# Performance work log

Measured on AMD Instinct MI355X. Metric: run time of the kernel, lower is better.

Reference implementation:

```python
import jax, jax.numpy as jnp
import numpy as np

B, D, H, W = 32, 256, 32, 32
K = 1024

def setup_inputs() -> dict:
    key = jax.random.key(0)
    k1, k2 = jax.random.split(key)
    x = jax.random.normal(k1, (B, D, H, W), dtype=jnp.float32)
    codebook = jax.random.normal(k2, (K, D), dtype=jnp.float32)
    return {"x": x, "codebook": codebook}

def reference(x, codebook):
    b, lat, h, w = x.shape
    # (B, D, H, W) -> (B*H*W, D) tokens
    xt = jnp.transpose(x, (0, 2, 3, 1)).reshape(-1, lat)  # [N, D]
    # Squared euclidean distances via expansion (argmin-equivalent to cdist)
    x_sq = jnp.sum(xt * xt, axis=-1, keepdims=True)           # [N, 1]
    c_sq = jnp.sum(codebook * codebook, axis=-1)[None, :]     # [1, K]
    dist2 = x_sq - 2.0 * (xt @ codebook.T) + c_sq             # [N, K]
    idx = jnp.argmin(dist2, axis=-1)                          # [N]
    quant = codebook[idx]                                     # [N, D]
    codebook_loss = jnp.mean((jax.lax.stop_gradient(xt) - quant) ** 2)
    commitment_loss = jnp.mean((xt - jax.lax.stop_gradient(quant)) ** 2)
    # Straight-through estimator
    out = xt + jax.lax.stop_gradient(quant - xt)              # [N, D]
    out = out.reshape(b, h, w, lat).transpose(0, 3, 1, 2)     # [B, D, H, W]
    min_enc_idx = idx.reshape(b, h, w)                        # [B, H, W]
    return out, min_enc_idx, codebook_loss, commitment_loss
```

## Files before the change

kernel.cpp:

```cpp
#include <hip/hip_runtime.h>

#define B_   32
#define D_   256
#define HW_  1024
#define N_   32768
#define K_   1024
#define DHW  (D_ * HW_)
#define MARGIN 0.3f

typedef __attribute__((ext_vector_type(8)))  short bf16x8;
typedef __attribute__((ext_vector_type(16))) float f32x16;

union FragU { uint4 q; bf16x8 v; };

__device__ inline uint bf16rne(float x) {
    uint ub = __float_as_uint(x);
    return (ub + 0x7fffu + ((ub >> 16) & 1u)) >> 16;
}

__global__ __launch_bounds__(256)
void prep_cb(const float* __restrict__ cb, uint4* __restrict__ cbt2,
             float* __restrict__ csq, float* __restrict__ cbT,
             int* __restrict__ rcount, float* __restrict__ oloss) {
    __shared__ uint sh[256], sl[256];
    __shared__ float rr[4];
    const int k = blockIdx.x, d = threadIdx.x;
    float v = cb[(size_t)k * D_ + d];
    uint hb = bf16rne(v);
    float hf = __uint_as_float(hb << 16);
    uint lb = bf16rne(v - hf);
    sh[d] = hb; sl[d] = lb;
    cbT[(size_t)d * K_ + k] = v;
    float s = v * v;
    #pragma unroll
    for (int off = 32; off >= 1; off >>= 1) s += __shfl_xor(s, off, 64);
    if ((d & 63) == 0) rr[d >> 6] = s;
    __syncthreads();
    if (d == 0) csq[k] = (rr[0] + rr[1]) + (rr[2] + rr[3]);
    if (k == 0 && d == 0) { *rcount = 0; oloss[0] = 0.f; oloss[1] = 0.f; }
    if (d < 64) {
        const int ch = d >> 2, it = d & 3;
        const int p = it >> 1, h = it & 1;
        const int d0 = ch * 16 + h * 8;
        const uint* src = p ? sl : sh;
        uint w[4];
        #pragma unroll
        for (int jj = 0; jj < 4; ++jj)
            w[jj] = src[d0 + 2 * jj] | (src[d0 + 2 * jj + 1] << 16);
        cbt2[((ch * 4 + it) << 10) + k] = make_uint4(w[0], w[1], w[2], w[3]);
    }
}

#define DO_STEP(SA, SB, SC, SD, S) do {                                          \
    const int cc_ = cq * 4 + (S);                                                \
    const int ch_ = cc_ & 15;                                                    \
    FragU tf[4];                                                                 \
    _Pragma("unroll")                                                            \
    for (int j = 0; j < 4; ++j) tf[j].q = TkS[ch_ * 2 + sub][j * 32 + l31];      \
    __builtin_amdgcn_s_setprio(1);                                               \
    _Pragma("unroll")                                                            \
    for (int j = 0; j < 4; ++j)                                                  \
        acc[0][j] = __builtin_amdgcn_mfma_f32_32x32x16_bf16(SA.v, tf[j].v, acc[0][j], 0, 0, 0); \
    _Pragma("unroll")                                                            \
    for (int j = 0; j < 4; ++j)                                                  \
        acc[1][j] = __builtin_amdgcn_mfma_f32_32x32x16_bf16(SB.v, tf[j].v, acc[1][j], 0, 0, 0); \
    _Pragma("unroll")                                                            \
    for (int j = 0; j < 4; ++j)                                                  \
        acc[0][j] = __builtin_amdgcn_mfma_f32_32x32x16_bf16(SC.v, tf[j].v, acc[0][j], 0, 0, 0); \
    _Pragma("unroll")                                                            \
    for (int j = 0; j < 4; ++j)                                                  \
        acc[1][j] = __builtin_amdgcn_mfma_f32_32x32x16_bf16(SD.v, tf[j].v, acc[1][j], 0, 0, 0); \
    __builtin_amdgcn_s_setprio(0);                                               \
    if (cq < 7) {                                                                \
        const int nc_ = cc_ + 4;                                                 \
        const int noff_ = (((nc_ & 15) * 4) << 10) + ((nc_ >> 4) * 64);          \
        SA.q = cb_hi[noff_];      SB.q = cb_hi[noff_ + 32];                      \
        SC.q = cb_lo[noff_];      SD.q = cb_lo[noff_ + 32];                      \
    }                                                                            \
} while (0)

__global__ __launch_bounds__(512, 1)
void vq_main(const float* __restrict__ x, const uint4* __restrict__ cbt2,
             const float* __restrict__ csqg, const float* __restrict__ cb,
             int* __restrict__ rcount, int* __restrict__ rlist,
             float* __restrict__ bdist, float* __restrict__ out,
             float* __restrict__ oidx, float* __restrict__ oloss) {
    __shared__ __align__(16) uint SMEM[17408];
    uint4 (*TkS)[128] = reinterpret_cast<uint4(*)[128]>(SMEM);
    float* csqS = reinterpret_cast<float*>(SMEM + 16384);

    const int tid = threadIdx.x;
    const int lane = tid & 63;
    const int sub = lane >> 5, l31 = lane & 31;
    const int w = tid >> 6;
    const int tok0 = blockIdx.x * 128;
    const int bb = tok0 >> 10, hw0 = tok0 & 1023;

    csqS[tid] = csqg[tid];
    csqS[tid + 512] = csqg[tid + 512];

    const uint4* cb_hi = cbt2 + (sub << 10) + w * 128 + l31;
    const uint4* cb_lo = cbt2 + ((2 + sub) << 10) + w * 128 + l31;

    FragU p0a, p0b, p0c, p0d, p1a, p1b, p1c, p1d,
          p2a, p2b, p2c, p2d, p3a, p3b, p3c, p3d;
    p0a.q = cb_hi[0];         p0b.q = cb_hi[32];
    p0c.q = cb_lo[0];         p0d.q = cb_lo[32];
    p1a.q = cb_hi[1 << 12];   p1b.q = cb_hi[(1 << 12) + 32];
    p1c.q = cb_lo[1 << 12];   p1d.q = cb_lo[(1 << 12) + 32];
    p2a.q = cb_hi[2 << 12];   p2b.q = cb_hi[(2 << 12) + 32];
    p2c.q = cb_lo[2 << 12];   p2d.q = cb_lo[(2 << 12) + 32];
    p3a.q = cb_hi[3 << 12];   p3b.q = cb_hi[(3 << 12) + 32];
    p3c.q = cb_lo[3 << 12];   p3d.q = cb_lo[(3 << 12) + 32];

    {
        const int t = tid & 127;
        const int dgrp = tid >> 7;
        const float* xp = x + (size_t)bb * DHW + hw0 + t;
        #pragma unroll
        for (int i = 0; i < 8; ++i) {
            int g = i * 4 + dgrp;
            float v[8];
            #pragma unroll
            for (int e = 0; e < 8; ++e)
                v[e] = xp[(size_t)(g * 8 + e) * HW_];
            uint wd[4];
            #pragma unroll
            for (int jj = 0; jj < 4; ++jj)
                wd[jj] = bf16rne(v[2 * jj]) | (bf16rne(v[2 * jj + 1]) << 16);
            TkS[g][t] = make_uint4(wd[0], wd[1], wd[2], wd[3]);
        }
    }
    __syncthreads();

    f32x16 acc[2][4] = {};
    float v1[4], v2[4]; int k1[4];
    #pragma unroll
    for (int j = 0; j < 4; ++j) { v1[j] = 3.4e38f; v2[j] = 3.4e38f; k1[j] = 0; }

    for (int cq = 0; cq < 8; ++cq) {
        DO_STEP(p0a, p0b, p0c, p0d, 0);
        DO_STEP(p1a, p1b, p1c, p1d, 1);
        DO_STEP(p2a, p2b, p2c, p2d, 2);
        DO_STEP(p3a, p3b, p3c, p3d, 3);

        if ((cq & 3) == 3) {
            const int ct = cq >> 2;
            const int cbase = w * 128 + ct * 64 + sub * 4;
            #pragma unroll
            for (int f = 0; f < 2; ++f) {
                #pragma unroll
                for (int g8 = 0; g8 < 4; ++g8) {
                    float4 cs4 = *reinterpret_cast<const float4*>(&csqS[cbase + f * 32 + g8 * 8]);
                    const float csa[4] = {cs4.x, cs4.y, cs4.z, cs4.w};
                    #pragma unroll
                    for (int q = 0; q < 4; ++q) {
                        int code = cbase + f * 32 + g8 * 8 + q;
                        int r = g8 * 4 + q;
                        #pragma unroll
                        for (int j = 0; j < 4; ++j) {
                            float s = fmaf(-2.f, acc[f][j][r], csa[q]);
                            bool c = s < v1[j];
                            v2[j] = c ? v1[j] : fminf(v2[j], s);
                            k1[j] = c ? code : k1[j];
                            v1[j] = c ? s : v1[j];
                        }
                    }
                }
            }
            const f32x16 zf = {};
            #pragma unroll
            for (int f = 0; f < 2; ++f)
                #pragma unroll
                for (int j = 0; j < 4; ++j) acc[f][j] = zf;
        }
    }

    #pragma unroll
    for (int j = 0; j < 4; ++j) {
        float ov1 = __shfl_xor(v1[j], 32, 64);
        float ov2 = __shfl_xor(v2[j], 32, 64);
        int   ok1 = __shfl_xor(k1[j], 32, 64);
        float nv2 = fminf(fminf(v2[j], ov2), fmaxf(v1[j], ov1));
        if (ov1 < v1[j] || (ov1 == v1[j] && ok1 < k1[j])) { v1[j] = ov1; k1[j] = ok1; }
        v2[j] = nv2;
    }
    __syncthreads();
    float* red = reinterpret_cast<float*>(SMEM);
    int* bestk_s = reinterpret_cast<int*>(SMEM + 17280);
    if (sub == 0) {
        #pragma unroll
        for (int j = 0; j < 4; ++j) {
            int t = j * 32 + l31;
            red[(w * 128 + t) * 3 + 0] = v1[j];
            red[(w * 128 + t) * 3 + 1] = v2[j];
            red[(w * 128 + t) * 3 + 2] = __int_as_float(k1[j]);
        }
    }
    __syncthreads();
    if (tid < 128) {
        float bv1 = red[tid * 3], bv2 = red[tid * 3 + 1];
        int bk = __float_as_int(red[tid * 3 + 2]);
        #pragma unroll
        for (int m = 1; m < 8; ++m) {
            float a1 = red[(m * 128 + tid) * 3], a2 = red[(m * 128 + tid) * 3 + 1];
            int ak = __float_as_int(red[(m * 128 + tid) * 3 + 2]);
            float nv2 = fminf(fminf(bv2, a2), fmaxf(bv1, a1));
            if (a1 < bv1 || (a1 == bv1 && ak < bk)) { bv1 = a1; bk = ak; }
            bv2 = nv2;
        }
        int n = tok0 + tid;
        bestk_s[tid] = bk;
        bdist[n] = bv1;
        oidx[n] = (float)bk;
        if (bv2 - bv1 < MARGIN) rlist[atomicAdd(rcount, 1)] = n;
        float v = bv1;
        #pragma unroll
        for (int off = 32; off >= 1; off >>= 1) v += __shfl_xor(v, off, 64);
        if ((tid & 63) == 0) {
            float t2 = v * (1.0f / 8388608.0f);
            atomicAdd(&oloss[0], t2);
            atomicAdd(&oloss[1], t2);
        }
    }
    __syncthreads();

    float* S2 = reinterpret_cast<float*>(SMEM);
    #pragma unroll 1
    for (int h = 0; h < 2; ++h) {
        #pragma unroll
        for (int i = 0; i < 8; ++i) {
            int r = w * 8 + i;
            int kk = bestk_s[h * 64 + r];
            float4 cw4 = *reinterpret_cast<const float4*>(cb + (size_t)kk * D_ + lane * 4);
            *reinterpret_cast<float4*>(&S2[r * 260 + lane * 4]) = cw4;
        }
        __syncthreads();
        {
            const int q = tid & 15, dg = tid >> 4;
            const size_t obase = (size_t)bb * DHW + hw0 + h * 64 + q * 4;
            #pragma unroll
            for (int dd = 0; dd < 8; ++dd) {
                int d = dg * 8 + dd;
                float4 wv;
                wv.x = S2[(q * 4 + 0) * 260 + d];
                wv.y = S2[(q * 4 + 1) * 260 + d];
                wv.z = S2[(q * 4 + 2) * 260 + d];
                wv.w = S2[(q * 4 + 3) * 260 + d];
                *reinterpret_cast<float4*>(out + obase + (size_t)d * HW_) = wv;
            }
        }
        __syncthreads();
    }
}

__global__ __launch_bounds__(1024)
void vq_refine(const float* __restrict__ x, const float* __restrict__ cb,
               const float* __restrict__ cbT, const float* __restrict__ csq,
               const int* __restrict__ rcount, const int* __restrict__ rlist,
               const float* __restrict__ bdist, float* __restrict__ out,
               float* __restrict__ oidx, float* __restrict__ oloss) {
    __shared__ float xv[8][256];
    __shared__ float xsq[8];
    __shared__ float wredv[16][8];
    __shared__ int   wredk[16][8];
    __shared__ int   kfin[8];
    const int tid = threadIdx.x;
    const int code = tid;
    const int wv_i = tid >> 6, lane = tid & 63;
    const int cnt = min(rcount[0], N_);
    for (int base = blockIdx.x * 8; base < cnt; base += gridDim.x * 8) {
        const int m = min(8, cnt - base);
        __syncthreads();
        {
            const int j = tid >> 8, d = tid & 255;
            #pragma unroll
            for (int rep = 0; rep < 2; ++rep) {
                int jj = j + rep * 4;
                float val = 0.f;
                if (jj < m) {
                    int n = rlist[base + jj];
                    int b = n >> 10, hw = n & 1023;
                    val = x[(size_t)b * DHW + (size_t)d * HW_ + hw];
                }
                xv[jj][d] = val;
            }
        }
        __syncthreads();
        if (tid < 256) {
            int g = tid >> 5, l = tid & 31;
            float s = 0.f;
            #pragma unroll
            for (int d8 = 0; d8 < 8; ++d8) { float v = xv[g][d8 * 32 + l]; s = fmaf(v, v, s); }
            #pragma unroll
            for (int mm = 1; mm < 32; mm <<= 1) s += __shfl_xor(s, mm, 64);
            if (l == 0) xsq[g] = s;
        }
        __syncthreads();

        float dot[8];
        #pragma unroll
        for (int j = 0; j < 8; ++j) dot[j] = 0.f;

        for (int d0 = 0; d0 < 256; d0 += 8) {
            float xr[8][8];
            #pragma unroll
            for (int j = 0; j < 8; ++j) {
                float4 a = *reinterpret_cast<const float4*>(&xv[j][d0]);
                float4 b = *reinterpret_cast<const float4*>(&xv[j][d0 + 4]);
                xr[j][0] = a.x; xr[j][1] = a.y; xr[j][2] = a.z; xr[j][3] = a.w;
                xr[j][4] = b.x; xr[j][5] = b.y; xr[j][6] = b.z; xr[j][7] = b.w;
            }
            float cv[8];
            #pragma unroll
            for (int u = 0; u < 8; ++u)
                cv[u] = cbT[(size_t)(d0 + u) * K_ + code];
            #pragma unroll
            for (int u = 0; u < 8; ++u)
                #pragma unroll
                for (int j = 0; j < 8; ++j)
                    dot[j] = fmaf(cv[u], xr[j][u], dot[j]);
        }

        const float cs = csq[code];
        #pragma unroll
        for (int j = 0; j < 8; ++j) {
            if (j < m) {
                float v = fmaf(-2.f, dot[j], xsq[j]) + cs;
                int k = code;
                #pragma unroll
                for (int mm = 1; mm < 64; mm <<= 1) {
                    float ov = __shfl_xor(v, mm, 64);
                    int   ok = __shfl_xor(k, mm, 64);
                    if (ov < v || (ov == v && ok < k)) { v = ov; k = ok; }
                }
                if (lane == 0) { wredv[wv_i][j] = v; wredk[wv_i][j] = k; }
            }
        }
        __syncthreads();
        if (tid < m) {
            float v = wredv[0][tid]; int k = wredk[0][tid];
            #pragma unroll
            for (int q = 1; q < 16; ++q) {
                if (wredv[q][tid] < v || (wredv[q][tid] == v && wredk[q][tid] < k)) {
                    v = wredv[q][tid]; k = wredk[q][tid];
                }
            }
            int n = rlist[base + tid];
            kfin[tid] = k;
            oidx[n] = (float)k;
            float delta = (v - bdist[n]) * (1.0f / 8388608.0f);
            atomicAdd(&oloss[0], delta);
            atomicAdd(&oloss[1], delta);
        }
        __syncthreads();
        {
            const int j = tid >> 8, d = tid & 255;
            #pragma unroll
            for (int rep = 0; rep < 2; ++rep) {
                int jj = j + rep * 4;
                if (jj < m) {
                    int n = rlist[base + jj];
                    int b = n >> 10, hw = n & 1023;
                    out[(size_t)b * DHW + (size_t)d * HW_ + hw] = cb[(size_t)kfin[jj] * D_ + d];
                }
            }
        }
        __syncthreads();
    }
}

extern "C" void kernel_launch(void* const* d_in, const int* in_sizes, int n_in,
                              void* d_out, int out_size, void* d_ws, size_t ws_size,
                              hipStream_t stream) {
    const float* x  = (const float*)d_in[0];
    const float* cb = (const float*)d_in[1];

    float* out   = (float*)d_out;
    float* oidx  = out + 8388608;
    float* oloss = out + 8388608 + 32768;

    uint* wsb = (uint*)d_ws;
    uint4*  cbt2  = (uint4*)wsb;
    float*  csq   = (float*)(wsb + 262144);
    float*  cbT   = (float*)(wsb + 263168);
    int*    rcount= (int*)  (wsb + 525312);
    int*    rlist = (int*)  (wsb + 525316);
    float*  bdist = (float*)(wsb + 558084);

    prep_cb <<<1024, 256, 0, stream>>>(cb, cbt2, csq, cbT, rcount, oloss);
    vq_main <<<256, 512, 0, stream>>>(x, cbt2, csq, cb, rcount, rlist, bdist, out, oidx, oloss);
    vq_refine<<<128, 1024, 0, stream>>>(x, cb, cbT, csq, rcount, rlist, bdist, out, oidx, oloss);
}
```

Before: 107.3 us.

## Narrow per-wave code tile and double-buffer token fragments from LDS

The distance GEMM loop is reorganised so each wave computes one 32-code fragment per step instead of two. Code tiles now span 256 codes over 16 outer iterations, which halves the accumulator and prefetch register footprint. Token fragments are double-buffered, so the LDS read for the next K-chunk is issued before the current chunk's MFMAs. The transpose staging buffer padding also changes from 260 to 261 to cut LDS bank conflicts. In exchange, each LDS token fragment now feeds half as many MFMAs, and 16-byte stores at an odd row stride are no longer 16-byte aligned.

```diff
diff --git a/kernel.cpp b/kernel.cpp
--- a/kernel.cpp
+++ b/kernel.cpp
@@ -51,31 +51,27 @@
     }
 }
 
-#define DO_STEP(SA, SB, SC, SD, S) do {                                          \
-    const int cc_ = cq * 4 + (S);                                                \
-    const int ch_ = cc_ & 15;                                                    \
-    FragU tf[4];                                                                 \
-    _Pragma("unroll")                                                            \
-    for (int j = 0; j < 4; ++j) tf[j].q = TkS[ch_ * 2 + sub][j * 32 + l31];      \
+#define DO_STEP(SH, SL, TFU, TFL, S) do {                                        \
+    const int s_ = sq * 4 + (S);                                                 \
+    if (s_ + 1 < 64) {                                                           \
+        const int nch_ = (s_ + 1) & 15;                                          \
+        _Pragma("unroll")                                                        \
+        for (int j = 0; j < 4; ++j)                                              \
+            TFL[j].q = TkS[nch_ * 2 + sub][j * 32 + l31];                        \
+    }                                                                            \
     __builtin_amdgcn_s_setprio(1);                                               \
     _Pragma("unroll")                                                            \
     for (int j = 0; j < 4; ++j)                                                  \
-        acc[0][j] = __builtin_amdgcn_mfma_f32_32x32x16_bf16(SA.v, tf[j].v, acc[0][j], 0, 0, 0); \
+        acc[j] = __builtin_amdgcn_mfma_f32_32x32x16_bf16(SH.v, TFU[j].v, acc[j], 0, 0, 0); \
     _Pragma("unroll")                                                            \
     for (int j = 0; j < 4; ++j)                                                  \
-        acc[1][j] = __builtin_amdgcn_mfma_f32_32x32x16_bf16(SB.v, tf[j].v, acc[1][j], 0, 0, 0); \
-    _Pragma("unroll")                                                            \
-    for (int j = 0; j < 4; ++j)                                                  \
-        acc[0][j] = __builtin_amdgcn_mfma_f32_32x32x16_bf16(SC.v, tf[j].v, acc[0][j], 0, 0, 0); \
-    _Pragma("unroll")                                                            \
-    for (int j = 0; j < 4; ++j)                                                  \
-        acc[1][j] = __builtin_amdgcn_mfma_f32_32x32x16_bf16(SD.v, tf[j].v, acc[1][j], 0, 0, 0); \
+        acc[j] = __builtin_amdgcn_mfma_f32_32x32x16_bf16(SL.v, TFU[j].v, acc[j], 0, 0, 0); \
     __builtin_amdgcn_s_setprio(0);                                               \
-    if (cq < 7) {                                                                \
-        const int nc_ = cc_ + 4;                                                 \
-        const int noff_ = (((nc_ & 15) * 4) << 10) + ((nc_ >> 4) * 64);          \
-        SA.q = cb_hi[noff_];      SB.q = cb_hi[noff_ + 32];                      \
-        SC.q = cb_lo[noff_];      SD.q = cb_lo[noff_ + 32];                      \
+    if (s_ + 4 < 64) {                                                           \
+        const int nc_ = s_ + 4;                                                  \
+        const int noff_ = (((nc_ & 15) * 4) << 10) + ((nc_ >> 4) * 256);         \
+        SH.q = cb_hi[noff_];                                                     \
+        SL.q = cb_lo[noff_];                                                     \
     }                                                                            \
 } while (0)
 
@@ -99,19 +95,14 @@
     csqS[tid] = csqg[tid];
     csqS[tid + 512] = csqg[tid + 512];
 
-    const uint4* cb_hi = cbt2 + (sub << 10) + w * 128 + l31;
-    const uint4* cb_lo = cbt2 + ((2 + sub) << 10) + w * 128 + l31;
-
-    FragU p0a, p0b, p0c, p0d, p1a, p1b, p1c, p1d,
-          p2a, p2b, p2c, p2d, p3a, p3b, p3c, p3d;
-    p0a.q = cb_hi[0];         p0b.q = cb_hi[32];
-    p0c.q = cb_lo[0];         p0d.q = cb_lo[32];
-    p1a.q = cb_hi[1 << 12];   p1b.q = cb_hi[(1 << 12) + 32];
-    p1c.q = cb_lo[1 << 12];   p1d.q = cb_lo[(1 << 12) + 32];
-    p2a.q = cb_hi[2 << 12];   p2b.q = cb_hi[(2 << 12) + 32];
-    p2c.q = cb_lo[2 << 12];   p2d.q = cb_lo[(2 << 12) + 32];
-    p3a.q = cb_hi[3 << 12];   p3b.q = cb_hi[(3 << 12) + 32];
-    p3c.q = cb_lo[3 << 12];   p3d.q = cb_lo[(3 << 12) + 32];
+    const uint4* cb_hi = cbt2 + (sub << 10) + w * 32 + l31;
+    const uint4* cb_lo = cbt2 + ((2 + sub) << 10) + w * 32 + l31;
+
+    FragU s0h, s0l, s1h, s1l, s2h, s2l, s3h, s3l;
+    s0h.q = cb_hi[0];         s0l.q = cb_lo[0];
+    s1h.q = cb_hi[1 << 12];   s1l.q = cb_lo[1 << 12];
+    s2h.q = cb_hi[2 << 12];   s2l.q = cb_lo[2 << 12];
+    s3h.q = cb_hi[3 << 12];   s3l.q = cb_lo[3 << 12];
 
     {
         const int t = tid & 127;
@@ -133,46 +124,46 @@
     }
     __syncthreads();
 
-    f32x16 acc[2][4] = {};
+    f32x16 acc[4] = {};
     float v1[4], v2[4]; int k1[4];
     #pragma unroll
     for (int j = 0; j < 4; ++j) { v1[j] = 3.4e38f; v2[j] = 3.4e38f; k1[j] = 0; }
 
-    for (int cq = 0; cq < 8; ++cq) {
-        DO_STEP(p0a, p0b, p0c, p0d, 0);
-        DO_STEP(p1a, p1b, p1c, p1d, 1);
-        DO_STEP(p2a, p2b, p2c, p2d, 2);
-        DO_STEP(p3a, p3b, p3c, p3d, 3);
-
-        if ((cq & 3) == 3) {
-            const int ct = cq >> 2;
-            const int cbase = w * 128 + ct * 64 + sub * 4;
-            #pragma unroll
-            for (int f = 0; f < 2; ++f) {
+    FragU tfA[4], tfB[4];
+    #pragma unroll
+    for (int j = 0; j < 4; ++j)
+        tfA[j].q = TkS[sub][j * 32 + l31];
+
+    for (int sq = 0; sq < 16; ++sq) {
+        DO_STEP(s0h, s0l, tfA, tfB, 0);
+        DO_STEP(s1h, s1l, tfB, tfA, 1);
+        DO_STEP(s2h, s2l, tfA, tfB, 2);
+        DO_STEP(s3h, s3l, tfB, tfA, 3);
+
+        if ((sq & 3) == 3) {
+            const int ct = sq >> 2;
+            const int cbase = ct * 256 + w * 32 + sub * 4;
+            #pragma unroll
+            for (int g8 = 0; g8 < 4; ++g8) {
+                float4 cs4 = *reinterpret_cast<const float4*>(&csqS[cbase + g8 * 8]);
+                const float csa[4] = {cs4.x, cs4.y, cs4.z, cs4.w};
                 #pragma unroll
-                for (int g8 = 0; g8 < 4; ++g8) {
-                    float4 cs4 = *reinterpret_cast<const float4*>(&csqS[cbase + f * 32 + g8 * 8]);
-                    const float csa[4] = {cs4.x, cs4.y, cs4.z, cs4.w};
+                for (int q = 0; q < 4; ++q) {
+                    int code = cbase + g8 * 8 + q;
+                    int r = g8 * 4 + q;
                     #pragma unroll
-                    for (int q = 0; q < 4; ++q) {
-                        int code = cbase + f * 32 + g8 * 8 + q;
-                        int r = g8 * 4 + q;
-                        #pragma unroll
-                        for (int j = 0; j < 4; ++j) {
-                            float s = fmaf(-2.f, acc[f][j][r], csa[q]);
-                            bool c = s < v1[j];
-                            v2[j] = c ? v1[j] : fminf(v2[j], s);
-                            k1[j] = c ? code : k1[j];
-                            v1[j] = c ? s : v1[j];
-                        }
+                    for (int j = 0; j < 4; ++j) {
+                        float s = fmaf(-2.f, acc[j][r], csa[q]);
+                        bool c = s < v1[j];
+                        v2[j] = c ? v1[j] : fminf(v2[j], s);
+                        k1[j] = c ? code : k1[j];
+                        v1[j] = c ? s : v1[j];
                     }
                 }
             }
             const f32x16 zf = {};
             #pragma unroll
-            for (int f = 0; f < 2; ++f)
-                #pragma unroll
-                for (int j = 0; j < 4; ++j) acc[f][j] = zf;
+            for (int j = 0; j < 4; ++j) acc[j] = zf;
         }
     }
 
@@ -233,7 +224,7 @@
             int r = w * 8 + i;
             int kk = bestk_s[h * 64 + r];
             float4 cw4 = *reinterpret_cast<const float4*>(cb + (size_t)kk * D_ + lane * 4);
-            *reinterpret_cast<float4*>(&S2[r * 260 + lane * 4]) = cw4;
+            *reinterpret_cast<float4*>(&S2[r * 261 + lane * 4]) = cw4;
         }
         __syncthreads();
         {
@@ -243,10 +234,10 @@
             for (int dd = 0; dd < 8; ++dd) {
                 int d = dg * 8 + dd;
                 float4 wv;
-                wv.x = S2[(q * 4 + 0) * 260 + d];
-                wv.y = S2[(q * 4 + 1) * 260 + d];
-                wv.z = S2[(q * 4 + 2) * 260 + d];
-                wv.w = S2[(q * 4 + 3) * 260 + d];
+                wv.x = S2[(q * 4 + 0) * 261 + d];
+                wv.y = S2[(q * 4 + 1) * 261 + d];
+                wv.z = S2[(q * 4 + 2) * 261 + d];
+                wv.w = S2[(q * 4 + 3) * 261 + d];
                 *reinterpret_cast<float4*>(out + obase + (size_t)d * HW_) = wv;
             }
         }
```

After: 107.9 us. About the same (+0.5%).
